# Kernel optimization log

Measured on AMD Instinct MI355X. Metric: run time of the kernel, lower is better.

## Reference

```python
import jax, jax.numpy as jnp
import numpy as np

VOCAB, EMB, HID, OUT = 4411, 64, 128, 2


def setup_inputs() -> dict:
    key = jax.random.key(0)
    ks = jax.random.split(key, 8)
    inputs = jax.random.randint(ks[0], (1024, 512), 0, VOCAB)
    s_e = 1.0
    s_ih = 1.0 / np.sqrt(HID)
    emb_table = jax.random.normal(ks[1], (VOCAB, EMB), dtype=jnp.float32) * s_e
    W_ih = jax.random.uniform(ks[2], (HID, EMB), dtype=jnp.float32, minval=-s_ih, maxval=s_ih)
    W_hh = jax.random.uniform(ks[3], (HID, HID), dtype=jnp.float32, minval=-s_ih, maxval=s_ih)
    b_ih = jax.random.uniform(ks[4], (HID,), dtype=jnp.float32, minval=-s_ih, maxval=s_ih)
    b_hh = jax.random.uniform(ks[5], (HID,), dtype=jnp.float32, minval=-s_ih, maxval=s_ih)
    s_l = 1.0 / np.sqrt(HID)
    W_lin = jax.random.uniform(ks[6], (OUT, HID), dtype=jnp.float32, minval=-s_l, maxval=s_l)
    b_lin = jax.random.uniform(ks[7], (OUT,), dtype=jnp.float32, minval=-s_l, maxval=s_l)
    return {"inputs": inputs, "emb_table": emb_table, "W_ih": W_ih, "W_hh": W_hh,
            "b_ih": b_ih, "b_hh": b_hh, "W_lin": W_lin, "b_lin": b_lin}


def reference(inputs, emb_table, W_ih, W_hh, b_ih, b_hh, W_lin, b_lin):
    # Embedding lookup: [B, T, EMB]
    emb = emb_table[inputs]
    B = emb.shape[0]
    # Precompute input projection for all timesteps: [B, T, HID]
    x_proj = jnp.einsum('bte,he->bth', emb, W_ih) + b_ih + b_hh
    h0 = jnp.zeros((B, W_hh.shape[0]), dtype=emb.dtype)

    def step(h, x_t):  # x_t: [B, HID]
        h_new = jnp.tanh(x_t + h @ W_hh.T)
        return h_new, None

    # scan over time axis
    h_final, _ = jax.lax.scan(step, h0, jnp.swapaxes(x_proj, 0, 1))
    # out_state squeeze(dim=0) -> [B, HID]; linear head -> [B, 2]
    return h_final @ W_lin.T + b_lin
```

## Files before the change

kernel.cpp:

```cpp
#include <hip/hip_runtime.h>
#include <hip/hip_bf16.h>


constexpr int Bc    = 1024;
constexpr int Tc    = 512;
constexpr int Ec    = 64;
constexpr int Hc    = 128;
constexpr int OUTc  = 2;
constexpr int VOCAB = 4411;

typedef short  short8  __attribute__((ext_vector_type(8)));
typedef float  floatx4 __attribute__((ext_vector_type(4)));

__device__ __forceinline__ unsigned short f2bf(float x) {
    union { __hip_bfloat16 h; unsigned short u; } v;
    v.h = __float2bfloat16(x);
    return v.u;
}
__device__ __forceinline__ float bf2f(unsigned short u) {
    union { float f; unsigned int u; } c;
    c.u = ((unsigned int)u) << 16;
    return c.f;
}
__device__ __forceinline__ unsigned int pack2bf(float lo, float hi) {
    union { __hip_bfloat162 h; unsigned int u; } c;
    c.h = __float22bfloat162_rn(float2{lo, hi});
    return c.u;
}
__device__ __forceinline__ float fast_tanh(float z) {
    const float e = __builtin_amdgcn_exp2f(2.8853900817779268f * z);
    return 1.0f - 2.0f * __builtin_amdgcn_rcpf(e + 1.0f);
}

#define LGKM_BARRIER() asm volatile("s_waitcnt lgkmcnt(0)\n\ts_barrier" ::: "memory")

__global__ __launch_bounds__(Hc) void pe_kernel(
    const float* __restrict__ emb, const float* __restrict__ W_ih,
    const float* __restrict__ b_ih, const float* __restrict__ b_hh,
    float* __restrict__ pe)
{
    const int v = blockIdx.x;
    const int j = threadIdx.x;
    const float* er = emb + (long)v * Ec;
    const float* wr = W_ih + j * Ec;
    float a0 = b_ih[j] + b_hh[j], a1 = 0.f, a2 = 0.f, a3 = 0.f;
#pragma unroll
    for (int e = 0; e < Ec; e += 4) {
        const float4 E = *(const float4*)(er + e);
        const float4 W = *(const float4*)(wr + e);
        a0 = fmaf(E.x, W.x, a0);
        a1 = fmaf(E.y, W.y, a1);
        a2 = fmaf(E.z, W.z, a2);
        a3 = fmaf(E.w, W.w, a3);
    }
    pe[(long)v * Hc + j] = (a0 + a1) + (a2 + a3);
}

constexpr int HT_BUF     = 2048;
constexpr int TOK_STRIDE = 513;

__global__ __attribute__((amdgpu_flat_work_group_size(256, 256)))
void rnn_mfma(
    const int*   __restrict__ inputs,
    const float* __restrict__ pe,
    const float* __restrict__ W_hh,
    const float* __restrict__ W_lin,
    const float* __restrict__ b_lin,
    float* __restrict__ out)
{
    const int tid = threadIdx.x;
    const int w   = tid >> 6;
    const int L   = tid & 63;
    const int q   = L >> 4;
    const int b   = L & 15;
    const int blk = blockIdx.x;
    const int jb  = w * 32;

    __shared__ __align__(16) unsigned short HT[2 * HT_BUF];
    __shared__ int toks[16 * TOK_STRIDE];

    {
        const int base = blk * 16 * Tc;
        for (int i = tid; i < 16 * Tc / 4; i += 256) {
            const int4 v4 = *(const int4*)(inputs + base + i * 4);
            const int bb = (i * 4) >> 9, t0 = (i * 4) & 511;
            int* dst = &toks[bb * TOK_STRIDE + t0];
            dst[0] = v4.x; dst[1] = v4.y; dst[2] = v4.z; dst[3] = v4.w;
        }
    }
    {
        unsigned int* z = (unsigned int*)HT;
        for (int i = tid; i < HT_BUF / 2; i += 256) z[i] = 0u;
    }

    short8 wfrag[2][4];
#pragma unroll
    for (int jt = 0; jt < 2; ++jt) {
        const float* wr = W_hh + (jb + jt * 16 + b) * Hc;
#pragma unroll
        for (int kt = 0; kt < 4; ++kt) {
            const float4 w0 = *(const float4*)(wr + kt * 32 + q * 8);
            const float4 w1 = *(const float4*)(wr + kt * 32 + q * 8 + 4);
            union { short8 s; unsigned short u[8]; } uf;
            uf.u[0] = f2bf(w0.x); uf.u[1] = f2bf(w0.y);
            uf.u[2] = f2bf(w0.z); uf.u[3] = f2bf(w0.w);
            uf.u[4] = f2bf(w1.x); uf.u[5] = f2bf(w1.y);
            uf.u[6] = f2bf(w1.z); uf.u[7] = f2bf(w1.w);
            wfrag[jt][kt] = uf.s;
        }
    }
#pragma unroll
    for (int jt = 0; jt < 2; ++jt)
        asm volatile("" : "+v"(wfrag[jt][0]), "+v"(wfrag[jt][1]),
                          "+v"(wfrag[jt][2]), "+v"(wfrag[jt][3]));

    unsigned short* const ht0 = HT;
    unsigned short* const ht1 = HT + HT_BUF;
    const int rd_base = L * 8;
    int wr_off[2];
#pragma unroll
    for (int jt = 0; jt < 2; ++jt) {
        const int j0 = jb + jt * 16 + q * 4;
        wr_off[jt] = ((j0 >> 5) << 9) + (((j0 >> 3) & 3) * 16 + b) * 8 + (j0 & 7);
    }

    const int* tr = &toks[b * TOK_STRIDE];

    __syncthreads();

    float4 xpc[2], xpn[2];
    {
        const int t0 = tr[0], t1 = tr[1];
#pragma unroll
        for (int jt = 0; jt < 2; ++jt) {
            xpc[jt] = *(const float4*)(pe + (long)t0 * Hc + jb + jt * 16 + q * 4);
            xpn[jt] = *(const float4*)(pe + (long)t1 * Hc + jb + jt * 16 + q * 4);
        }
    }

    for (int t = 0; t < Tc; ++t) {
        unsigned short* const rbuf = (t & 1) ? ht1 : ht0;
        unsigned short* const wbuf = (t & 1) ? ht0 : ht1;

        short8 bfrag[4];
#pragma unroll
        for (int kt = 0; kt < 4; ++kt)
            bfrag[kt] = *(const short8*)(rbuf + kt * 512 + rd_base);

        float4 xp2[2];
        {
            const int tk = tr[(t + 2 < Tc) ? (t + 2) : (Tc - 1)];
#pragma unroll
            for (int jt = 0; jt < 2; ++jt)
                xp2[jt] = *(const float4*)(pe + (long)tk * Hc + jb + jt * 16 + q * 4);
        }

        floatx4 acc[2];
        acc[0] = (floatx4){xpc[0].x, xpc[0].y, xpc[0].z, xpc[0].w};
        acc[1] = (floatx4){xpc[1].x, xpc[1].y, xpc[1].z, xpc[1].w};
#pragma unroll
        for (int kt = 0; kt < 4; ++kt) {
            acc[0] = __builtin_amdgcn_mfma_f32_16x16x32_bf16(
                wfrag[0][kt], bfrag[kt], acc[0], 0, 0, 0);
            acc[1] = __builtin_amdgcn_mfma_f32_16x16x32_bf16(
                wfrag[1][kt], bfrag[kt], acc[1], 0, 0, 0);
        }

#pragma unroll
        for (int jt = 0; jt < 2; ++jt) {
            const float h0 = fast_tanh(acc[jt][0]);
            const float h1 = fast_tanh(acc[jt][1]);
            const float h2 = fast_tanh(acc[jt][2]);
            const float h3 = fast_tanh(acc[jt][3]);
            uint2 pk;
            pk.x = pack2bf(h0, h1);
            pk.y = pack2bf(h2, h3);
            *(uint2*)(wbuf + wr_off[jt]) = pk;
        }

        LGKM_BARRIER();

        xpc[0] = xpn[0]; xpc[1] = xpn[1];
        xpn[0] = xp2[0]; xpn[1] = xp2[1];
    }

    if (tid < 16 * OUTc) {
        const int bb = tid >> 1, o = tid & 1;
        float s = b_lin[o];
        const float* wl = W_lin + o * Hc;
#pragma unroll 8
        for (int k = 0; k < Hc; ++k) {
            const int off = ((k >> 5) << 9) + (((k >> 3) & 3) * 16 + bb) * 8 + (k & 7);
            s = fmaf(bf2f(ht0[off]), wl[k], s);
        }
        out[(blk * 16 + bb) * OUTc + o] = s;
    }
}

extern "C" void kernel_launch(void* const* d_in, const int* in_sizes, int n_in,
                              void* d_out, int out_size, void* d_ws, size_t ws_size,
                              hipStream_t stream) {
    const int*   inputs    = (const int*)d_in[0];
    const float* emb_table = (const float*)d_in[1];
    const float* W_ih      = (const float*)d_in[2];
    const float* W_hh      = (const float*)d_in[3];
    const float* b_ih      = (const float*)d_in[4];
    const float* b_hh      = (const float*)d_in[5];
    const float* W_lin     = (const float*)d_in[6];
    const float* b_lin     = (const float*)d_in[7];
    float* out = (float*)d_out;

    float* pe = (float*)d_ws;
    pe_kernel<<<VOCAB, Hc, 0, stream>>>(emb_table, W_ih, b_ih, b_hh, pe);
    rnn_mfma<<<Bc / 16, 256, 0, stream>>>(inputs, pe, W_hh, W_lin, b_lin, out);
}
```

Measured before the change: 281.5 us.

## Split RNN step across 8 waves and break MFMA dependency chain

The recurrent kernel now runs with 512 threads per block, so each of 8 waves owns 16 hidden units instead of 32, halving each wave's MFMA work per timestep. The four chained MFMAs are also split into two independent accumulator chains that are summed before tanh, which shortens the serial latency of each step. The aim is to cut per-step critical-path latency in this latency-bound recurrence, at the cost of a wider barrier across 8 waves each timestep and twice as many waves loading xp values.

```diff
diff --git a/kernel.cpp b/kernel.cpp
--- a/kernel.cpp
+++ b/kernel.cpp
@@ -59,7 +59,7 @@
 constexpr int HT_BUF     = 2048;
 constexpr int TOK_STRIDE = 513;
 
-__global__ __attribute__((amdgpu_flat_work_group_size(256, 256)))
+__global__ __attribute__((amdgpu_flat_work_group_size(512, 512)))
 void rnn_mfma(
     const int*   __restrict__ inputs,
     const float* __restrict__ pe,
@@ -74,14 +74,14 @@
     const int q   = L >> 4;
     const int b   = L & 15;
     const int blk = blockIdx.x;
-    const int jb  = w * 32;
+    const int jb  = w * 16;
 
     __shared__ __align__(16) unsigned short HT[2 * HT_BUF];
     __shared__ int toks[16 * TOK_STRIDE];
 
     {
         const int base = blk * 16 * Tc;
-        for (int i = tid; i < 16 * Tc / 4; i += 256) {
+        for (int i = tid; i < 16 * Tc / 4; i += 512) {
             const int4 v4 = *(const int4*)(inputs + base + i * 4);
             const int bb = (i * 4) >> 9, t0 = (i * 4) & 511;
             int* dst = &toks[bb * TOK_STRIDE + t0];
@@ -90,13 +90,12 @@
     }
     {
         unsigned int* z = (unsigned int*)HT;
-        for (int i = tid; i < HT_BUF / 2; i += 256) z[i] = 0u;
+        for (int i = tid; i < HT_BUF / 2; i += 512) z[i] = 0u;
     }
 
-    short8 wfrag[2][4];
-#pragma unroll
-    for (int jt = 0; jt < 2; ++jt) {
-        const float* wr = W_hh + (jb + jt * 16 + b) * Hc;
+    short8 wfrag[4];
+    {
+        const float* wr = W_hh + (jb + b) * Hc;
 #pragma unroll
         for (int kt = 0; kt < 4; ++kt) {
             const float4 w0 = *(const float4*)(wr + kt * 32 + q * 8);
@@ -106,36 +105,29 @@
             uf.u[2] = f2bf(w0.z); uf.u[3] = f2bf(w0.w);
             uf.u[4] = f2bf(w1.x); uf.u[5] = f2bf(w1.y);
             uf.u[6] = f2bf(w1.z); uf.u[7] = f2bf(w1.w);
-            wfrag[jt][kt] = uf.s;
+            wfrag[kt] = uf.s;
         }
     }
-#pragma unroll
-    for (int jt = 0; jt < 2; ++jt)
-        asm volatile("" : "+v"(wfrag[jt][0]), "+v"(wfrag[jt][1]),
-                          "+v"(wfrag[jt][2]), "+v"(wfrag[jt][3]));
+    asm volatile("" : "+v"(wfrag[0]), "+v"(wfrag[1]),
+                      "+v"(wfrag[2]), "+v"(wfrag[3]));
 
     unsigned short* const ht0 = HT;
     unsigned short* const ht1 = HT + HT_BUF;
     const int rd_base = L * 8;
-    int wr_off[2];
-#pragma unroll
-    for (int jt = 0; jt < 2; ++jt) {
-        const int j0 = jb + jt * 16 + q * 4;
-        wr_off[jt] = ((j0 >> 5) << 9) + (((j0 >> 3) & 3) * 16 + b) * 8 + (j0 & 7);
-    }
+    const int j0     = jb + q * 4;
+    const int wr_off = ((j0 >> 5) << 9) + (((j0 >> 3) & 3) * 16 + b) * 8 + (j0 & 7);
+    const int xp_off = jb + q * 4;
 
     const int* tr = &toks[b * TOK_STRIDE];
+    const floatx4 zac = (floatx4){0.f, 0.f, 0.f, 0.f};
 
     __syncthreads();
 
-    float4 xpc[2], xpn[2];
+    float4 xpc, xpn;
     {
         const int t0 = tr[0], t1 = tr[1];
-#pragma unroll
-        for (int jt = 0; jt < 2; ++jt) {
-            xpc[jt] = *(const float4*)(pe + (long)t0 * Hc + jb + jt * 16 + q * 4);
-            xpn[jt] = *(const float4*)(pe + (long)t1 * Hc + jb + jt * 16 + q * 4);
-        }
+        xpc = *(const float4*)(pe + (long)t0 * Hc + xp_off);
+        xpn = *(const float4*)(pe + (long)t1 * Hc + xp_off);
     }
 
     for (int t = 0; t < Tc; ++t) {
@@ -147,41 +139,31 @@
         for (int kt = 0; kt < 4; ++kt)
             bfrag[kt] = *(const short8*)(rbuf + kt * 512 + rd_base);
 
-        float4 xp2[2];
+        float4 xp2;
         {
             const int tk = tr[(t + 2 < Tc) ? (t + 2) : (Tc - 1)];
-#pragma unroll
-            for (int jt = 0; jt < 2; ++jt)
-                xp2[jt] = *(const float4*)(pe + (long)tk * Hc + jb + jt * 16 + q * 4);
+            xp2 = *(const float4*)(pe + (long)tk * Hc + xp_off);
         }
 
-        floatx4 acc[2];
-        acc[0] = (floatx4){xpc[0].x, xpc[0].y, xpc[0].z, xpc[0].w};
-        acc[1] = (floatx4){xpc[1].x, xpc[1].y, xpc[1].z, xpc[1].w};
-#pragma unroll
-        for (int kt = 0; kt < 4; ++kt) {
-            acc[0] = __builtin_amdgcn_mfma_f32_16x16x32_bf16(
-                wfrag[0][kt], bfrag[kt], acc[0], 0, 0, 0);
-            acc[1] = __builtin_amdgcn_mfma_f32_16x16x32_bf16(
-                wfrag[1][kt], bfrag[kt], acc[1], 0, 0, 0);
-        }
+        floatx4 acc0 = (floatx4){xpc.x, xpc.y, xpc.z, xpc.w};
+        acc0 = __builtin_amdgcn_mfma_f32_16x16x32_bf16(wfrag[0], bfrag[0], acc0, 0, 0, 0);
+        floatx4 acc1 = __builtin_amdgcn_mfma_f32_16x16x32_bf16(wfrag[2], bfrag[2], zac, 0, 0, 0);
+        acc0 = __builtin_amdgcn_mfma_f32_16x16x32_bf16(wfrag[1], bfrag[1], acc0, 0, 0, 0);
+        acc1 = __builtin_amdgcn_mfma_f32_16x16x32_bf16(wfrag[3], bfrag[3], acc1, 0, 0, 0);
 
-#pragma unroll
-        for (int jt = 0; jt < 2; ++jt) {
-            const float h0 = fast_tanh(acc[jt][0]);
-            const float h1 = fast_tanh(acc[jt][1]);
-            const float h2 = fast_tanh(acc[jt][2]);
-            const float h3 = fast_tanh(acc[jt][3]);
-            uint2 pk;
-            pk.x = pack2bf(h0, h1);
-            pk.y = pack2bf(h2, h3);
-            *(uint2*)(wbuf + wr_off[jt]) = pk;
-        }
+        const float h0 = fast_tanh(acc0[0] + acc1[0]);
+        const float h1 = fast_tanh(acc0[1] + acc1[1]);
+        const float h2 = fast_tanh(acc0[2] + acc1[2]);
+        const float h3 = fast_tanh(acc0[3] + acc1[3]);
+        uint2 pk;
+        pk.x = pack2bf(h0, h1);
+        pk.y = pack2bf(h2, h3);
+        *(uint2*)(wbuf + wr_off) = pk;
 
         LGKM_BARRIER();
 
-        xpc[0] = xpn[0]; xpc[1] = xpn[1];
-        xpn[0] = xp2[0]; xpn[1] = xp2[1];
+        xpc = xpn;
+        xpn = xp2;
     }
 
     if (tid < 16 * OUTc) {
@@ -212,5 +194,5 @@
 
     float* pe = (float*)d_ws;
     pe_kernel<<<VOCAB, Hc, 0, stream>>>(emb_table, W_ih, b_ih, b_hh, pe);
-    rnn_mfma<<<Bc / 16, 256, 0, stream>>>(inputs, pe, W_hh, W_lin, b_lin, out);
+    rnn_mfma<<<Bc / 16, 512, 0, stream>>>(inputs, pe, W_hh, W_lin, b_lin, out);
 }
```

Measured after the change: 245.5 us. 1.15x faster.

## Fuse input projection into recurrent MFMA kernel and split hidden-state accumulation chain

Applied to the files above, without the earlier changes.

Drops the separate vocab-wide projection kernel and computes the input projection for each step inside the RNN loop with bf16 MFMAs from the prefetched embedding rows, keeping W_ih fragments in registers. Embedding rows are prefetched three steps ahead and the next step's projection is computed while the current recurrence runs. The recurrent MFMA chain is split into two independent accumulators to shorten the dependent latency per step. This removes one launch and the projection-table write and read, but adds MFMA work and registers inside the serial loop and rounds the input projection through bf16.

```diff
diff --git a/kernel.cpp b/kernel.cpp
--- a/kernel.cpp
+++ b/kernel.cpp
@@ -7,7 +7,6 @@
 constexpr int Ec    = 64;
 constexpr int Hc    = 128;
 constexpr int OUTc  = 2;
-constexpr int VOCAB = 4411;
 
 typedef short  short8  __attribute__((ext_vector_type(8)));
 typedef float  floatx4 __attribute__((ext_vector_type(4)));
@@ -27,6 +26,14 @@
     c.h = __float22bfloat162_rn(float2{lo, hi});
     return c.u;
 }
+__device__ __forceinline__ short8 cvt8bf(float4 a, float4 b) {
+    union { short8 s; unsigned int u[4]; } r;
+    r.u[0] = pack2bf(a.x, a.y);
+    r.u[1] = pack2bf(a.z, a.w);
+    r.u[2] = pack2bf(b.x, b.y);
+    r.u[3] = pack2bf(b.z, b.w);
+    return r.s;
+}
 __device__ __forceinline__ float fast_tanh(float z) {
     const float e = __builtin_amdgcn_exp2f(2.8853900817779268f * z);
     return 1.0f - 2.0f * __builtin_amdgcn_rcpf(e + 1.0f);
@@ -34,36 +41,16 @@
 
 #define LGKM_BARRIER() asm volatile("s_waitcnt lgkmcnt(0)\n\ts_barrier" ::: "memory")
 
-__global__ __launch_bounds__(Hc) void pe_kernel(
-    const float* __restrict__ emb, const float* __restrict__ W_ih,
-    const float* __restrict__ b_ih, const float* __restrict__ b_hh,
-    float* __restrict__ pe)
-{
-    const int v = blockIdx.x;
-    const int j = threadIdx.x;
-    const float* er = emb + (long)v * Ec;
-    const float* wr = W_ih + j * Ec;
-    float a0 = b_ih[j] + b_hh[j], a1 = 0.f, a2 = 0.f, a3 = 0.f;
-#pragma unroll
-    for (int e = 0; e < Ec; e += 4) {
-        const float4 E = *(const float4*)(er + e);
-        const float4 W = *(const float4*)(wr + e);
-        a0 = fmaf(E.x, W.x, a0);
-        a1 = fmaf(E.y, W.y, a1);
-        a2 = fmaf(E.z, W.z, a2);
-        a3 = fmaf(E.w, W.w, a3);
-    }
-    pe[(long)v * Hc + j] = (a0 + a1) + (a2 + a3);
-}
-
 constexpr int HT_BUF     = 2048;
 constexpr int TOK_STRIDE = 513;
 
-__global__ __attribute__((amdgpu_flat_work_group_size(256, 256)))
-void rnn_mfma(
+__global__ __launch_bounds__(256, 1) void rnn_fused(
     const int*   __restrict__ inputs,
-    const float* __restrict__ pe,
+    const float* __restrict__ emb,
+    const float* __restrict__ W_ih,
     const float* __restrict__ W_hh,
+    const float* __restrict__ b_ih,
+    const float* __restrict__ b_hh,
     const float* __restrict__ W_lin,
     const float* __restrict__ b_lin,
     float* __restrict__ out)
@@ -98,21 +85,32 @@
     for (int jt = 0; jt < 2; ++jt) {
         const float* wr = W_hh + (jb + jt * 16 + b) * Hc;
 #pragma unroll
-        for (int kt = 0; kt < 4; ++kt) {
-            const float4 w0 = *(const float4*)(wr + kt * 32 + q * 8);
-            const float4 w1 = *(const float4*)(wr + kt * 32 + q * 8 + 4);
-            union { short8 s; unsigned short u[8]; } uf;
-            uf.u[0] = f2bf(w0.x); uf.u[1] = f2bf(w0.y);
-            uf.u[2] = f2bf(w0.z); uf.u[3] = f2bf(w0.w);
-            uf.u[4] = f2bf(w1.x); uf.u[5] = f2bf(w1.y);
-            uf.u[6] = f2bf(w1.z); uf.u[7] = f2bf(w1.w);
-            wfrag[jt][kt] = uf.s;
-        }
+        for (int kt = 0; kt < 4; ++kt)
+            wfrag[jt][kt] = cvt8bf(*(const float4*)(wr + kt * 32 + q * 8),
+                                   *(const float4*)(wr + kt * 32 + q * 8 + 4));
+    }
+    short8 ifrag[2][2];
+#pragma unroll
+    for (int jt = 0; jt < 2; ++jt) {
+        const float* wr = W_ih + (jb + jt * 16 + b) * Ec;
+#pragma unroll
+        for (int et = 0; et < 2; ++et)
+            ifrag[jt][et] = cvt8bf(*(const float4*)(wr + et * 32 + q * 8),
+                                   *(const float4*)(wr + et * 32 + q * 8 + 4));
+    }
+    float4 biasv[2];
+#pragma unroll
+    for (int jt = 0; jt < 2; ++jt) {
+        const int j0 = jb + jt * 16 + q * 4;
+        const float4 bi = *(const float4*)(b_ih + j0);
+        const float4 bh = *(const float4*)(b_hh + j0);
+        biasv[jt] = float4{bi.x + bh.x, bi.y + bh.y, bi.z + bh.z, bi.w + bh.w};
     }
 #pragma unroll
     for (int jt = 0; jt < 2; ++jt)
         asm volatile("" : "+v"(wfrag[jt][0]), "+v"(wfrag[jt][1]),
-                          "+v"(wfrag[jt][2]), "+v"(wfrag[jt][3]));
+                          "+v"(wfrag[jt][2]), "+v"(wfrag[jt][3]),
+                          "+v"(ifrag[jt][0]), "+v"(ifrag[jt][1]));
 
     unsigned short* const ht0 = HT;
     unsigned short* const ht1 = HT + HT_BUF;
@@ -125,17 +123,36 @@
     }
 
     const int* tr = &toks[b * TOK_STRIDE];
+    const int e0 = q * 8;
+    const floatx4 zac = (floatx4){0.f, 0.f, 0.f, 0.f};
 
     __syncthreads();
 
-    float4 xpc[2], xpn[2];
+    floatx4 xz_cur[2];
+    float4  eload[4];
+    int     tk;
     {
         const int t0 = tr[0], t1 = tr[1];
+        tk = tr[2];
+        const float* er0 = emb + (long)t0 * Ec;
+        float4 ea = *(const float4*)(er0 + e0);
+        float4 eb = *(const float4*)(er0 + e0 + 4);
+        float4 ec = *(const float4*)(er0 + 32 + e0);
+        float4 ed = *(const float4*)(er0 + 32 + e0 + 4);
+        const short8 f0 = cvt8bf(ea, eb);
+        const short8 f1 = cvt8bf(ec, ed);
 #pragma unroll
         for (int jt = 0; jt < 2; ++jt) {
-            xpc[jt] = *(const float4*)(pe + (long)t0 * Hc + jb + jt * 16 + q * 4);
-            xpn[jt] = *(const float4*)(pe + (long)t1 * Hc + jb + jt * 16 + q * 4);
-        }
+            floatx4 a = (floatx4){biasv[jt].x, biasv[jt].y, biasv[jt].z, biasv[jt].w};
+            a = __builtin_amdgcn_mfma_f32_16x16x32_bf16(ifrag[jt][0], f0, a, 0, 0, 0);
+            a = __builtin_amdgcn_mfma_f32_16x16x32_bf16(ifrag[jt][1], f1, a, 0, 0, 0);
+            xz_cur[jt] = a;
+        }
+        const float* er1 = emb + (long)t1 * Ec;
+        eload[0] = *(const float4*)(er1 + e0);
+        eload[1] = *(const float4*)(er1 + e0 + 4);
+        eload[2] = *(const float4*)(er1 + 32 + e0);
+        eload[3] = *(const float4*)(er1 + 32 + e0 + 4);
     }
 
     for (int t = 0; t < Tc; ++t) {
@@ -147,31 +164,44 @@
         for (int kt = 0; kt < 4; ++kt)
             bfrag[kt] = *(const short8*)(rbuf + kt * 512 + rd_base);
 
-        float4 xp2[2];
+        const int tknew = tr[(t + 3 < Tc) ? (t + 3) : (Tc - 1)];
+        float4 enew[4];
         {
-            const int tk = tr[(t + 2 < Tc) ? (t + 2) : (Tc - 1)];
-#pragma unroll
-            for (int jt = 0; jt < 2; ++jt)
-                xp2[jt] = *(const float4*)(pe + (long)tk * Hc + jb + jt * 16 + q * 4);
-        }
-
-        floatx4 acc[2];
-        acc[0] = (floatx4){xpc[0].x, xpc[0].y, xpc[0].z, xpc[0].w};
-        acc[1] = (floatx4){xpc[1].x, xpc[1].y, xpc[1].z, xpc[1].w};
-#pragma unroll
-        for (int kt = 0; kt < 4; ++kt) {
-            acc[0] = __builtin_amdgcn_mfma_f32_16x16x32_bf16(
-                wfrag[0][kt], bfrag[kt], acc[0], 0, 0, 0);
-            acc[1] = __builtin_amdgcn_mfma_f32_16x16x32_bf16(
-                wfrag[1][kt], bfrag[kt], acc[1], 0, 0, 0);
+            const float* er = emb + (long)tk * Ec;
+            enew[0] = *(const float4*)(er + e0);
+            enew[1] = *(const float4*)(er + e0 + 4);
+            enew[2] = *(const float4*)(er + 32 + e0);
+            enew[3] = *(const float4*)(er + 32 + e0 + 4);
+        }
+
+        floatx4 xz_next[2];
+        {
+            const short8 f0 = cvt8bf(eload[0], eload[1]);
+            const short8 f1 = cvt8bf(eload[2], eload[3]);
+#pragma unroll
+            for (int jt = 0; jt < 2; ++jt) {
+                floatx4 a = (floatx4){biasv[jt].x, biasv[jt].y, biasv[jt].z, biasv[jt].w};
+                a = __builtin_amdgcn_mfma_f32_16x16x32_bf16(ifrag[jt][0], f0, a, 0, 0, 0);
+                a = __builtin_amdgcn_mfma_f32_16x16x32_bf16(ifrag[jt][1], f1, a, 0, 0, 0);
+                xz_next[jt] = a;
+            }
         }
 
 #pragma unroll
         for (int jt = 0; jt < 2; ++jt) {
-            const float h0 = fast_tanh(acc[jt][0]);
-            const float h1 = fast_tanh(acc[jt][1]);
-            const float h2 = fast_tanh(acc[jt][2]);
-            const float h3 = fast_tanh(acc[jt][3]);
+            floatx4 a0 = __builtin_amdgcn_mfma_f32_16x16x32_bf16(
+                wfrag[jt][0], bfrag[0], xz_cur[jt], 0, 0, 0);
+            floatx4 a1 = __builtin_amdgcn_mfma_f32_16x16x32_bf16(
+                wfrag[jt][2], bfrag[2], zac, 0, 0, 0);
+            a0 = __builtin_amdgcn_mfma_f32_16x16x32_bf16(
+                wfrag[jt][1], bfrag[1], a0, 0, 0, 0);
+            a1 = __builtin_amdgcn_mfma_f32_16x16x32_bf16(
+                wfrag[jt][3], bfrag[3], a1, 0, 0, 0);
+
+            const float h0 = fast_tanh(a0[0] + a1[0]);
+            const float h1 = fast_tanh(a0[1] + a1[1]);
+            const float h2 = fast_tanh(a0[2] + a1[2]);
+            const float h3 = fast_tanh(a0[3] + a1[3]);
             uint2 pk;
             pk.x = pack2bf(h0, h1);
             pk.y = pack2bf(h2, h3);
@@ -180,8 +210,10 @@
 
         LGKM_BARRIER();
 
-        xpc[0] = xpn[0]; xpc[1] = xpn[1];
-        xpn[0] = xp2[0]; xpn[1] = xp2[1];
+        xz_cur[0] = xz_next[0]; xz_cur[1] = xz_next[1];
+        eload[0] = enew[0]; eload[1] = enew[1];
+        eload[2] = enew[2]; eload[3] = enew[3];
+        tk = tknew;
     }
 
     if (tid < 16 * OUTc) {
@@ -210,7 +242,6 @@
     const float* b_lin     = (const float*)d_in[7];
     float* out = (float*)d_out;
 
-    float* pe = (float*)d_ws;
-    pe_kernel<<<VOCAB, Hc, 0, stream>>>(emb_table, W_ih, b_ih, b_hh, pe);
-    rnn_mfma<<<Bc / 16, 256, 0, stream>>>(inputs, pe, W_hh, W_lin, b_lin, out);
-}
+    rnn_fused<<<Bc / 16, 256, 0, stream>>>(inputs, emb_table, W_ih, W_hh,
+                                           b_ih, b_hh, W_lin, b_lin, out);
+}
```

New measurement: 370.6 us. 31.6% more time.
